# Optimization experiments

Hardware: AMD Instinct MI355X
Metric: run time of the kernel (lower is better)

The kernel has to match this reference:

```python
import jax, jax.numpy as jnp
import numpy as np

NEG = -1e30  # finite stand-in for -inf (keeps grads nan-free)
BLANK = 0


def _ctc_nll(log_probs, targets, input_lengths, target_lengths):
    """Per-sample CTC negative log-likelihood.
    log_probs: (B,T,V) log-softmax outputs; targets: (B,S) int; lengths: (B,)."""
    B, T, V = log_probs.shape
    S = targets.shape[1]
    L = 2 * S + 1
    # extended label sequence: blank, y1, blank, y2, ..., blank -> (B, L)
    ext = jnp.full((B, L), BLANK, dtype=targets.dtype).at[:, 1::2].set(targets)
    # skip transition (l-2 -> l) allowed iff ext[l] != blank and ext[l] != ext[l-2]
    prev2 = jnp.pad(ext[:, :-2], ((0, 0), (2, 0)), constant_values=-1)
    skip = (ext != BLANK) & (ext != prev2)  # (B, L)

    def emit(lp_t):  # lp_t: (B,V) -> (B,L)
        return jnp.take_along_axis(lp_t, ext, axis=1)

    alpha0 = jnp.where(jnp.arange(L)[None, :] < 2, emit(log_probs[:, 0]), NEG)

    def step(alpha, lp_t):
        p1 = jnp.pad(alpha[:, :-1], ((0, 0), (1, 0)), constant_values=NEG)
        p2 = jnp.pad(alpha[:, :-2], ((0, 0), (2, 0)), constant_values=NEG)
        p2 = jnp.where(skip, p2, NEG)
        m = jnp.maximum(alpha, jnp.maximum(p1, p2))
        lse = m + jnp.log(jnp.exp(alpha - m) + jnp.exp(p1 - m) + jnp.exp(p2 - m))
        new = lse + emit(lp_t)
        return new, new

    # scan over time; collect alphas so we can read them at each sample's T_b-1
    _, alphas_rest = jax.lax.scan(step, alpha0, jnp.swapaxes(log_probs, 0, 1)[1:])
    alphas = jnp.concatenate([alpha0[None], alphas_rest], axis=0)  # (T,B,L)
    alphas = jnp.swapaxes(alphas, 0, 1)  # (B,T,L)
    alpha_T = jnp.take_along_axis(
        alphas, (input_lengths - 1)[:, None, None], axis=1)[:, 0]  # (B,L)

    end1 = jnp.take_along_axis(alpha_T, (2 * target_lengths)[:, None], axis=1)[:, 0]
    end2 = jnp.take_along_axis(alpha_T, (2 * target_lengths - 1)[:, None], axis=1)[:, 0]
    m = jnp.maximum(end1, end2)
    ll = m + jnp.log(jnp.exp(end1 - m) + jnp.exp(end2 - m))
    return -ll  # (B,)


def setup_inputs() -> dict:
    key = jax.random.key(0)
    k1, k2, k3, k4 = jax.random.split(key, 4)
    B, T, V, S = 32, 2000, 1024, 256
    log_probs = jax.nn.log_softmax(
        jax.random.normal(k1, (B, T, V), dtype=jnp.float32), axis=-1)
    targets = jax.random.randint(k2, (B, S), 1, V)  # exclude blank=0
    input_lengths = jax.random.randint(k3, (B,), 1500, T + 1)
    target_lengths = jax.random.randint(k4, (B,), 128, S + 1)
    return {"log_probs": log_probs, "targets": targets,
            "input_lengths": input_lengths, "target_lengths": target_lengths}


def reference(log_probs, targets, input_lengths, target_lengths):
    nll = _ctc_nll(log_probs, targets, input_lengths, target_lengths)
    # zero_infinity=True: drop infeasible samples
    nll = jnp.where(nll > 0.5 * (-NEG), 0.0, nll)
    # reduction='mean': divide each loss by its target length, then batch-mean
    return jnp.mean(nll / target_lengths.astype(nll.dtype))
```

## Files before the change

### kernel.cpp

```cpp
#include <hip/hip_runtime.h>
#include <stdint.h>


#define LN2F 0.69314718055994530942f
#define PD 16

__device__ __forceinline__ float shr1f(float x) {
  return __int_as_float(
      __builtin_amdgcn_update_dpp(0, __float_as_int(x), 0x138, 0xF, 0xF, true));
}
__device__ __forceinline__ int shr1i(int x) {
  return __builtin_amdgcn_update_dpp(0, x, 0x138, 0xF, 0xF, true);
}

__global__ __launch_bounds__(256) void k_gather_exp(
    const float* __restrict__ lp, const int* __restrict__ tgt,
    const int* __restrict__ ilen, float* __restrict__ El,
    float* __restrict__ Eb, int T, int V, int S) {
  const int b = blockIdx.y;
  const int t = blockIdx.x;
  if (t >= ilen[b]) return;
  const int tid = threadIdx.x;
  const int lab = tgt[b * S + tid];
  const float* row = lp + ((size_t)b * T + t) * V;
  El[((size_t)b * T + t) * S + tid] = __expf(row[lab]);
  if (tid == 0) Eb[(size_t)b * T + t] = __expf(row[0]);
}

__global__ __launch_bounds__(64) void k_ctc_alpha(
    const float* __restrict__ El, const float* __restrict__ Eb,
    const int* __restrict__ tgt, const int* __restrict__ ilen,
    const int* __restrict__ tlen, float* __restrict__ nll_out, int T, int S) {
  const int b = blockIdx.x;
  const int lane = threadIdx.x;
  const bool l0 = (lane == 0);

  const int Tb = ilen[b];
  const int U = tlen[b];

  const int4 tg = *(const int4*)(tgt + (size_t)b * S + 4 * lane);
  const int tprev = __shfl_up(tg.w, 1);
  const float sk0 = (l0 || tg.x != tprev) ? 1.0f : 0.0f;
  const float sk1 = (tg.y != tg.x) ? 1.0f : 0.0f;
  const float sk2 = (tg.z != tg.y) ? 1.0f : 0.0f;
  const float sk3 = (tg.w != tg.z) ? 1.0f : 0.0f;

  const float* Elb = El + (size_t)b * T * 256;
  const float* Ebb = Eb + (size_t)b * T;

  float a0 = l0 ? Ebb[0] : 0.0f;
  float aL0 = l0 ? Elb[0] : 0.0f;
  float aL1 = 0, aL2 = 0, aL3 = 0;
  float aB0 = 0, aB1 = 0, aB2 = 0, aB3 = 0;
  int o = 0;
  float s = 1.0f;

  auto stepf = [&](float4 el, float eb) {
    float pL = shr1f(aL3) * s;
    float pB = shr1f(aB3) * s;
    pL = l0 ? 0.0f : pL;
    pB = l0 ? a0 : pB;
    const float nB0 = (aB0 + aL0) * eb;
    const float nB1 = (aB1 + aL1) * eb;
    const float nB2 = (aB2 + aL2) * eb;
    const float nB3 = (aB3 + aL3) * eb;
    const float nL0 = (aL0 + fmaf(sk0, pL, pB)) * el.x;
    const float nL1 = (aL1 + fmaf(sk1, aL0, aB0)) * el.y;
    const float nL2 = (aL2 + fmaf(sk2, aL1, aB1)) * el.z;
    const float nL3 = (aL3 + fmaf(sk3, aL2, aB2)) * el.w;
    a0 *= eb;
    aL0 = nL0; aL1 = nL1; aL2 = nL2; aL3 = nL3;
    aB0 = nB0; aB1 = nB1; aB2 = nB2; aB3 = nB3;
  };
  auto renorm = [&]() {
    float m = fmaxf(fmaxf(fmaxf(aL0, aL1), fmaxf(aL2, aL3)),
                    fmaxf(fmaxf(aB0, aB1), fmaxf(aB2, aB3)));
    m = fmaxf(m, a0);
    const bool nz = (m > 0.0f);
    const int mk = nz ? (((__float_as_int(m) >> 23) & 0xff) - 126) : 0;
    const int ocand = o + mk;
    const int oleft = shr1i(ocand);
    o = (nz || l0) ? ocand : oleft;
    const float sc = nz ? __int_as_float((127 - mk) << 23) : 1.0f;
    aL0 *= sc; aL1 *= sc; aL2 *= sc; aL3 *= sc;
    aB0 *= sc; aB1 *= sc; aB2 *= sc; aB3 *= sc;
    a0 *= sc;
    int d = shr1i(o) - o;
    d = max(-126, min(126, d));
    s = __int_as_float((d + 127) << 23);
  };

  float4 pel[PD];
  float peb[PD];
  const int lo4 = 4 * lane;

#pragma unroll
  for (int j = 0; j < PD; ++j) {
    const int row = min(j + 1, Tb - 1);
    pel[j] = *(const float4*)(Elb + ((size_t)row << 8) + lo4);
    peb[j] = Ebb[row];
  }

  const int R = Tb - 1;
  const int nfull = R >> 4;
  const int rem = R & 15;

  for (int k = 0; k < nfull; ++k) {
    const int base = 1 + (k << 4);
#pragma unroll
    for (int j = 0; j < PD; ++j) {
      const float4 el = pel[j];
      const float eb = peb[j];
      const int row = min(base + PD + j, Tb - 1);
      pel[j] = *(const float4*)(Elb + ((size_t)row << 8) + lo4);
      peb[j] = Ebb[row];
      stepf(el, eb);
      if ((j & 3) == 2) renorm();
    }
  }
  {
#pragma unroll
    for (int j = 0; j < PD; ++j) {
      if (j < rem) {
        stepf(pel[j], peb[j]);
        if ((j & 3) == 2) renorm();
      }
    }
  }

  if (lane == ((U - 1) >> 2)) {
    const int j = (U - 1) & 3;
    float sv;
    if (j == 0)      sv = aL0 + aB0;
    else if (j == 1) sv = aL1 + aB1;
    else if (j == 2) sv = aL2 + aB2;
    else             sv = aL3 + aB3;
    float nll = -LN2F * (__log2f(sv) + (float)o);
    if (!(nll < 5e29f)) nll = 0.0f;
    nll_out[b] = nll / (float)U;
  }
}

__global__ __launch_bounds__(64) void k_reduce(const float* __restrict__ nll,
                                               float* __restrict__ out,
                                               int B) {
  float v = 0.0f;
  for (int i = threadIdx.x; i < B; i += 64) v += nll[i];
  for (int off = 32; off > 0; off >>= 1) v += __shfl_down(v, off);
  if (threadIdx.x == 0) out[0] = v / (float)B;
}

extern "C" void kernel_launch(void* const* d_in, const int* in_sizes, int n_in,
                              void* d_out, int out_size, void* d_ws,
                              size_t ws_size, hipStream_t stream) {
  const float* lp = (const float*)d_in[0];
  const int* tgt = (const int*)d_in[1];
  const int* ilen = (const int*)d_in[2];
  const int* tlen = (const int*)d_in[3];

  const int B = in_sizes[2];
  const int S = in_sizes[1] / B;
  const int V = 1024;
  const int T = (int)((size_t)in_sizes[0] / ((size_t)B * V));

  float* El = (float*)d_ws;
  float* Eb = El + (size_t)B * T * S;
  float* nw = Eb + (size_t)B * T;

  dim3 g1(T, B);
  k_gather_exp<<<g1, 256, 0, stream>>>(lp, tgt, ilen, El, Eb, T, V, S);
  k_ctc_alpha<<<B, 64, 0, stream>>>(El, Eb, tgt, ilen, tlen, nw, T, S);
  k_reduce<<<1, 64, 0, stream>>>(nw, (float*)d_out, B);
}
```

Baseline: 514.4 us.

## Batch gather over 8 timesteps per block and macro-unroll alpha prefetch pipeline

Each gather block now processes 8 consecutive timesteps, issuing all loads before the exps and cutting the block count by a factor of 8. The alpha recursion's prefetch ring is rewritten as 16 named scalar registers via macros, so the compiler keeps it in registers rather than possibly in scratch. It also adds launch_bounds(64,1). The aim is to reduce gather launch/block overhead and keep the serial alpha loop's prefetch fully in VGPRs, at the cost of less gather parallelism and more register pressure.

```diff
diff --git a/kernel.cpp b/kernel.cpp
--- a/kernel.cpp
+++ b/kernel.cpp
@@ -4,6 +4,10 @@
 
 #define LN2F 0.69314718055994530942f
 #define PD 16
+#define CH 8
+
+#define X16(M) M(0) M(1) M(2) M(3) M(4) M(5) M(6) M(7) \
+               M(8) M(9) M(10) M(11) M(12) M(13) M(14) M(15)
 
 __device__ __forceinline__ float shr1f(float x) {
   return __int_as_float(
@@ -18,16 +22,35 @@
     const int* __restrict__ ilen, float* __restrict__ El,
     float* __restrict__ Eb, int T, int V, int S) {
   const int b = blockIdx.y;
-  const int t = blockIdx.x;
-  if (t >= ilen[b]) return;
+  const int Tb = ilen[b];
+  const int t0 = blockIdx.x * CH;
+  if (t0 >= Tb) return;
   const int tid = threadIdx.x;
   const int lab = tgt[b * S + tid];
-  const float* row = lp + ((size_t)b * T + t) * V;
-  El[((size_t)b * T + t) * S + tid] = __expf(row[lab]);
-  if (tid == 0) Eb[(size_t)b * T + t] = __expf(row[0]);
+  const float* rb = lp + (size_t)b * T * V;
+  const int nr = min(CH, Tb - t0);
+
+  if (nr == CH) {
+    float v[CH];
+#pragma unroll
+    for (int j = 0; j < CH; ++j)
+      v[j] = rb[(size_t)(t0 + j) * V + lab];
+    const float bl = (tid < CH) ? rb[(size_t)(t0 + tid) * V] : 0.0f;
+#pragma unroll
+    for (int j = 0; j < CH; ++j)
+      El[((size_t)b * T + t0 + j) * 256 + tid] = __expf(v[j]);
+    if (tid < CH) Eb[(size_t)b * T + t0 + tid] = __expf(bl);
+  } else {
+#pragma unroll
+    for (int j = 0; j < CH; ++j)
+      if (j < nr)
+        El[((size_t)b * T + t0 + j) * 256 + tid] =
+            __expf(rb[(size_t)(t0 + j) * V + lab]);
+    if (tid < nr) Eb[(size_t)b * T + t0 + tid] = __expf(rb[(size_t)(t0 + tid) * V]);
+  }
 }
 
-__global__ __launch_bounds__(64) void k_ctc_alpha(
+__global__ __launch_bounds__(64, 1) void k_ctc_alpha(
     const float* __restrict__ El, const float* __restrict__ Eb,
     const int* __restrict__ tgt, const int* __restrict__ ilen,
     const int* __restrict__ tlen, float* __restrict__ nll_out, int T, int S) {
@@ -37,6 +60,7 @@
 
   const int Tb = ilen[b];
   const int U = tlen[b];
+  const int Tbm1 = Tb - 1;
 
   const int4 tg = *(const int4*)(tgt + (size_t)b * S + 4 * lane);
   const int tprev = __shfl_up(tg.w, 1);
@@ -90,43 +114,37 @@
     s = __int_as_float((d + 127) << 23);
   };
 
-  float4 pel[PD];
-  float peb[PD];
   const int lo4 = 4 * lane;
 
-#pragma unroll
-  for (int j = 0; j < PD; ++j) {
-    const int row = min(j + 1, Tb - 1);
-    pel[j] = *(const float4*)(Elb + ((size_t)row << 8) + lo4);
-    peb[j] = Ebb[row];
-  }
+#define PIPE_DECL(j) float4 P##j; float Q##j;
+  X16(PIPE_DECL)
 
-  const int R = Tb - 1;
+#define PIPE_LOAD(j) {                                                  \
+    const int r_ = min((j) + 1, Tbm1);                                  \
+    P##j = *(const float4*)(Elb + ((size_t)r_ << 8) + lo4);             \
+    Q##j = Ebb[r_]; }
+  X16(PIPE_LOAD)
+
+  const int R = Tbm1;
   const int nfull = R >> 4;
   const int rem = R & 15;
 
   for (int k = 0; k < nfull; ++k) {
     const int base = 1 + (k << 4);
-#pragma unroll
-    for (int j = 0; j < PD; ++j) {
-      const float4 el = pel[j];
-      const float eb = peb[j];
-      const int row = min(base + PD + j, Tb - 1);
-      pel[j] = *(const float4*)(Elb + ((size_t)row << 8) + lo4);
-      peb[j] = Ebb[row];
-      stepf(el, eb);
-      if ((j & 3) == 2) renorm();
-    }
+#define PIPE_STEP(j) {                                                  \
+      const float4 el_ = P##j;                                          \
+      const float eb_ = Q##j;                                           \
+      const int r_ = min(base + PD + (j), Tbm1);                        \
+      P##j = *(const float4*)(Elb + ((size_t)r_ << 8) + lo4);           \
+      Q##j = Ebb[r_];                                                   \
+      stepf(el_, eb_);                                                  \
+      if (((j) & 3) == 2) renorm(); }
+    X16(PIPE_STEP)
   }
-  {
-#pragma unroll
-    for (int j = 0; j < PD; ++j) {
-      if (j < rem) {
-        stepf(pel[j], peb[j]);
-        if ((j & 3) == 2) renorm();
-      }
-    }
-  }
+#define PIPE_TAIL(j) if ((j) < rem) {                                   \
+    stepf(P##j, Q##j);                                                  \
+    if (((j) & 3) == 2) renorm(); }
+  X16(PIPE_TAIL)
 
   if (lane == ((U - 1) >> 2)) {
     const int j = (U - 1) & 3;
@@ -167,7 +185,7 @@
   float* Eb = El + (size_t)B * T * S;
   float* nw = Eb + (size_t)B * T;
 
-  dim3 g1(T, B);
+  dim3 g1((T + CH - 1) / CH, B);
   k_gather_exp<<<g1, 256, 0, stream>>>(lp, tgt, ilen, El, Eb, T, V, S);
   k_ctc_alpha<<<B, 64, 0, stream>>>(El, Eb, tgt, ilen, tlen, nw, T, S);
   k_reduce<<<1, 64, 0, stream>>>(nw, (float*)d_out, B);
```

New measurement: 548.9 us. +6.7%, slower.
